# Optimization experiments

Measured on AMD Instinct MI355X. Metric: run time of the kernel, lower is better.

Reference implementation:

```python
import jax, jax.numpy as jnp
import numpy as np

SIGMA = 1.0
EPS = 1e-5
NEG = 0.1
CPG = 16  # channels_per_group


def bn(x, g, b):
    # batch norm over the point dimension (training-mode batch stats)
    m = x.mean(0, keepdims=True)
    v = x.var(0, keepdims=True)
    return (x - m) / jnp.sqrt(v + EPS) * g + b


def lrelu(x):
    return jnp.where(x >= 0, x, NEG * x)


def kpinv_conv(q_pts, s_pts, x, idx, kp, w_g1, b_g1, w_g2, b_g2):
    # KPInv: neighbor gather + kernel-point influence weighting + dynamically
    # generated (involution-style) per-point, per-kernel, per-group weights.
    M, H = idx.shape
    K = kp.shape[0]
    C = x.shape[1]
    G = C // CPG
    # shadow padding: far-away point, zero feature
    s_pts_p = jnp.concatenate([s_pts, jnp.full((1, s_pts.shape[1]), 1e6, s_pts.dtype)], 0)
    x_p = jnp.concatenate([x, jnp.zeros((1, C), x.dtype)], 0)
    npts = s_pts_p[idx] - q_pts[:, None, :]              # (M,H,D) relative neighbor positions
    nfeat = x_p[idx]                                      # (M,H,C) gathered neighbor features
    # squared distances to kernel points without materializing (M,H,K,D)
    d2 = ((npts ** 2).sum(-1)[:, :, None]
          + (kp ** 2).sum(-1)[None, None, :]
          - 2.0 * jnp.einsum('mhd,kd->mhk', npts, kp))    # (M,H,K)
    # linear influence, sum aggregation
    infl = jnp.clip(1.0 - jnp.sqrt(jnp.maximum(d2, 0.0)) / SIGMA, 0.0, None)
    fk = jnp.einsum('mhk,mhc->mkc', infl, nfeat)          # (M,K,C) per-kernel aggregated feats
    # generate conv weights from local max-pooled center feature
    center = jnp.max(nfeat, axis=1)                       # (M,C)
    w = lrelu(center @ w_g1 + b_g1) @ w_g2 + b_g2         # (M,K*G)
    w = w.reshape(M, K, G)
    fk = fk.reshape(M, K, G, CPG)
    return jnp.einsum('mkg,mkgc->mgc', w, fk).reshape(M, C)


def setup_inputs() -> dict:
    key = jax.random.key(0)
    ks = jax.random.split(key, 10)
    M, H, Cin, Cmid, K, D = 50000, 32, 128, 32, 15, 3
    R = 2.5
    pts = jax.random.uniform(ks[0], (M, D), dtype=jnp.float32) * 10.0
    return dict(
        q_pts=pts,
        s_pts=pts,
        s_feats=jax.random.normal(ks[1], (M, Cin), dtype=jnp.float32),
        neighbor_indices=jax.random.randint(ks[2], (M, H), 0, M),
        kernel_points=jax.random.normal(ks[3], (K, D), dtype=jnp.float32) * (0.3 * R),
        w_u1=jax.random.normal(ks[4], (Cin, Cmid), dtype=jnp.float32) / np.float32(np.sqrt(Cin)),
        g_u1=jnp.ones((Cmid,), jnp.float32), b_u1=jnp.zeros((Cmid,), jnp.float32),
        w_g1=jax.random.normal(ks[5], (Cmid, Cmid // 4), dtype=jnp.float32) / np.float32(np.sqrt(Cmid)),
        b_g1=jnp.zeros((Cmid // 4,), jnp.float32),
        w_g2=jax.random.normal(ks[6], (Cmid // 4, K * (Cmid // CPG)), dtype=jnp.float32) / np.float32(np.sqrt(Cmid // 4)),
        b_g2=jnp.zeros((K * (Cmid // CPG),), jnp.float32),
        g_c=jnp.ones((Cmid,), jnp.float32), b_c=jnp.zeros((Cmid,), jnp.float32),
        w_u2=jax.random.normal(ks[7], (Cmid, Cin), dtype=jnp.float32) / np.float32(np.sqrt(Cmid)),
        g_u2=jnp.ones((Cin,), jnp.float32), b_u2=jnp.zeros((Cin,), jnp.float32),
    )


def reference(q_pts, s_pts, s_feats, neighbor_indices, kernel_points,
              w_u1, g_u1, b_u1, w_g1, b_g1, w_g2, b_g2,
              g_c, b_c, w_u2, g_u2, b_u2):
    # unary1: linear -> BN -> LeakyReLU (in_channels != mid_channels)
    x = lrelu(bn(s_feats @ w_u1, g_u1, b_u1))
    # KPInv conv block: conv -> BN -> LeakyReLU
    x = kpinv_conv(q_pts, s_pts, x, neighbor_indices, kernel_points, w_g1, b_g1, w_g2, b_g2)
    x = lrelu(bn(x, g_c, b_c))
    # unary2: linear -> BN (no activation)
    x = bn(x @ w_u2, g_u2, b_u2)
    # not strided, in==out: shortcut is identity on s_feats
    return lrelu(x + s_feats)
```

## Files before the change

kernel.cpp:

```cpp
#include <hip/hip_runtime.h>

#define CMID 32
#define CIN 128
#define HNB 32
#define KP 15
#define NEG 0.1f
#define EPS 1e-5f

__global__ __launch_bounds__(256) void k1_gemm1(
    const float* __restrict__ A,
    const float* __restrict__ B,
    float* __restrict__ y1,
    float* __restrict__ st,
    int M)
{
    __shared__ __align__(16) float AsT[32 * 128];
    __shared__ __align__(16) float Bs[128 * 32];
    __shared__ __align__(16) float red[256];
    int t = threadIdx.x;
    for (int i = t; i < 128 * 32; i += 256) Bs[i] = B[i];

    int m0 = blockIdx.x * 128;
    int tx = t & 7, ty = t >> 3;
    int srow = t & 127, shh = t >> 7;
    float acc[4][4] = {{0.f}};

    for (int ch = 0; ch < 4; ++ch) {
        __syncthreads();
        int gr = m0 + srow;
        const float4* ap = (const float4*)(A + (size_t)gr * CIN + ch * 32 + shh * 16);
        float4 f0, f1, f2, f3;
        if (gr < M) { f0 = ap[0]; f1 = ap[1]; f2 = ap[2]; f3 = ap[3]; }
        else { f0 = f1 = f2 = f3 = make_float4(0.f, 0.f, 0.f, 0.f); }
        {
            int cb = shh * 16;
            AsT[(cb + 0) * 128 + srow] = f0.x;  AsT[(cb + 1) * 128 + srow] = f0.y;
            AsT[(cb + 2) * 128 + srow] = f0.z;  AsT[(cb + 3) * 128 + srow] = f0.w;
            AsT[(cb + 4) * 128 + srow] = f1.x;  AsT[(cb + 5) * 128 + srow] = f1.y;
            AsT[(cb + 6) * 128 + srow] = f1.z;  AsT[(cb + 7) * 128 + srow] = f1.w;
            AsT[(cb + 8) * 128 + srow] = f2.x;  AsT[(cb + 9) * 128 + srow] = f2.y;
            AsT[(cb + 10) * 128 + srow] = f2.z; AsT[(cb + 11) * 128 + srow] = f2.w;
            AsT[(cb + 12) * 128 + srow] = f3.x; AsT[(cb + 13) * 128 + srow] = f3.y;
            AsT[(cb + 14) * 128 + srow] = f3.z; AsT[(cb + 15) * 128 + srow] = f3.w;
        }
        __syncthreads();
        const float* bsp = Bs + (ch * 32) * 32 + tx * 4;
#pragma unroll
        for (int jl = 0; jl < 32; ++jl) {
            float4 av = *(const float4*)(AsT + jl * 128 + ty * 4);
            float4 bv = *(const float4*)(bsp + jl * 32);
            acc[0][0] += av.x * bv.x; acc[0][1] += av.x * bv.y; acc[0][2] += av.x * bv.z; acc[0][3] += av.x * bv.w;
            acc[1][0] += av.y * bv.x; acc[1][1] += av.y * bv.y; acc[1][2] += av.y * bv.z; acc[1][3] += av.y * bv.w;
            acc[2][0] += av.z * bv.x; acc[2][1] += av.z * bv.y; acc[2][2] += av.z * bv.z; acc[2][3] += av.z * bv.w;
            acc[3][0] += av.w * bv.x; acc[3][1] += av.w * bv.y; acc[3][2] += av.w * bv.z; acc[3][3] += av.w * bv.w;
        }
    }
#pragma unroll
    for (int i = 0; i < 4; ++i) {
        int r = m0 + ty * 4 + i;
        if (r < M)
            *(float4*)(y1 + (size_t)r * CMID + tx * 4) =
                make_float4(acc[i][0], acc[i][1], acc[i][2], acc[i][3]);
    }
    float s4[4], q4[4];
#pragma unroll
    for (int e = 0; e < 4; ++e) {
        s4[e] = acc[0][e] + acc[1][e] + acc[2][e] + acc[3][e];
        q4[e] = acc[0][e] * acc[0][e] + acc[1][e] * acc[1][e]
              + acc[2][e] * acc[2][e] + acc[3][e] * acc[3][e];
    }
#pragma unroll
    for (int off = 8; off <= 32; off <<= 1) {
#pragma unroll
        for (int e = 0; e < 4; ++e) {
            s4[e] += __shfl_xor(s4[e], off);
            q4[e] += __shfl_xor(q4[e], off);
        }
    }
    int lw = t >> 6, ll = t & 63;
    if (ll < 8) {
#pragma unroll
        for (int e = 0; e < 4; ++e) {
            red[(lw * 8 + ll) * 8 + e] = s4[e];
            red[(lw * 8 + ll) * 8 + 4 + e] = q4[e];
        }
    }
    __syncthreads();
    if (t < 64) {
        int tx2 = t >> 3, k = t & 7;
        float v = red[(0 * 8 + tx2) * 8 + k] + red[(1 * 8 + tx2) * 8 + k]
                + red[(2 * 8 + tx2) * 8 + k] + red[(3 * 8 + tx2) * 8 + k];
        int col = tx2 * 4 + (k & 3);
        atomicAdd(&st[(k < 4 ? 0 : 32) + col], v);
    }
}

__global__ __launch_bounds__(256, 4) void k3_kpinv(
    const float* __restrict__ y1, const float* __restrict__ st,
    const float* __restrict__ q_pts, const float* __restrict__ s_pts,
    const int* __restrict__ idx, const float* __restrict__ kp,
    const float* __restrict__ g_u1, const float* __restrict__ b_u1,
    const float* __restrict__ w_g1, const float* __restrict__ b_g1,
    const float* __restrict__ w_g2, const float* __restrict__ b_g2,
    float* __restrict__ x2, int M)
{
    __shared__ __align__(16) float a1s[32], b1s[32];
    __shared__ __align__(16) float wg1[32 * 8];
    __shared__ __align__(16) float bg1[8];
    __shared__ __align__(16) float wg2[8 * 30];
    __shared__ __align__(16) float bg2[32];
    __shared__ __align__(16) float kps[KP * 3 + 1];
    __shared__ __align__(16) float vbuf[4][2][32 * 32];
    __shared__ __align__(16) float aux[4][2][144];

    int t = threadIdx.x;
    if (t < 32) {
        float mean = st[t] * (1.0f / M);
        float var  = st[32 + t] * (1.0f / M) - mean * mean;
        float inv  = rsqrtf(var + EPS);
        float a = g_u1[t] * inv;
        a1s[t] = a;
        b1s[t] = b_u1[t] - mean * a;
    }
    wg1[t & 255] = w_g1[t & 255];
    if (t < 8)   bg1[t] = b_g1[t];
    if (t < 240) wg2[t] = w_g2[t];
    if (t < 30)  bg2[t] = b_g2[t];
    else if (t < 32) bg2[t] = 0.f;
    if (t < KP * 3) kps[t] = kp[t];
    __syncthreads();

    int wave = t >> 6, lane = t & 63;
    int p = lane >> 5;
    int q = lane & 31;
    int m = blockIdx.x * 8 + wave * 2 + p;
    bool valid = (m < M);
    int mm = valid ? m : 0;
    float* vb = &vbuf[wave][p][0];
    float* ax = &aux[wave][p][0];

    int h = q;
    int n = idx[(size_t)mm * HNB + h];
    float qx = q_pts[mm * 3 + 0], qy = q_pts[mm * 3 + 1], qz = q_pts[mm * 3 + 2];
    float dx = s_pts[n * 3 + 0] - qx;
    float dy = s_pts[n * 3 + 1] - qy;
    float dz = s_pts[n * 3 + 2] - qz;

    float infl[KP];
#pragma unroll
    for (int k = 0; k < KP; ++k) {
        float ex = dx - kps[k * 3 + 0];
        float ey = dy - kps[k * 3 + 1];
        float ez = dz - kps[k * 3 + 2];
        float d = sqrtf(ex * ex + ey * ey + ez * ez);
        infl[k] = fmaxf(1.0f - d, 0.f);
    }

    {
        const float4* row = (const float4*)(y1 + (size_t)n * CMID);
        int hq4 = h >> 2, h3 = h & 3;
#pragma unroll
        for (int jj = 0; jj < 8; ++jj) {
            float4 f = row[jj];
            float vv[4] = {f.x, f.y, f.z, f.w};
#pragma unroll
            for (int e = 0; e < 4; ++e) {
                int c = jj * 4 + e;
                float x = vv[e] * a1s[c] + b1s[c];
                x = fmaxf(x, NEG * x);
                vb[(c << 5) + ((hq4 ^ (c & 7)) << 2) + h3] = x;
            }
        }
    }
    __builtin_amdgcn_wave_barrier();

    {
        int c = q;
        int c7 = c & 7;
        const float* vrow = vb + (c << 5);
        float cm = -1e30f;
#pragma unroll
        for (int j = 0; j < 8; ++j) {
            const float4 f = *(const float4*)(vrow + ((j ^ c7) << 2));
            cm = fmaxf(fmaxf(fmaxf(cm, f.x), fmaxf(f.y, f.z)), f.w);
        }
        ax[c] = cm;
        __builtin_amdgcn_wave_barrier();

        int jm = c & 7;
        float acc = bg1[jm];
#pragma unroll
        for (int cc = 0; cc < 8; ++cc) {
            const float4 ce = *(const float4*)(ax + (cc << 2));
            acc += ce.x * wg1[(cc * 4 + 0) * 8 + jm];
            acc += ce.y * wg1[(cc * 4 + 1) * 8 + jm];
            acc += ce.z * wg1[(cc * 4 + 2) * 8 + jm];
            acc += ce.w * wg1[(cc * 4 + 3) * 8 + jm];
        }
        float h1v = fmaxf(acc, NEG * acc);
        if (c < 8) ax[32 + c] = h1v;
        __builtin_amdgcn_wave_barrier();

        float wv = 0.f;
        if (c < 30) {
            const float4 ha = *(const float4*)(ax + 32);
            const float4 hb = *(const float4*)(ax + 36);
            wv = bg2[c]
               + ha.x * wg2[0 * 30 + c] + ha.y * wg2[1 * 30 + c]
               + ha.z * wg2[2 * 30 + c] + ha.w * wg2[3 * 30 + c]
               + hb.x * wg2[4 * 30 + c] + hb.y * wg2[5 * 30 + c]
               + hb.z * wg2[6 * 30 + c] + hb.w * wg2[7 * 30 + c];
        }
        ax[40 + c] = wv;
    }
    __builtin_amdgcn_wave_barrier();

    {
        float wf[32];
#pragma unroll
        for (int j = 0; j < 8; ++j) {
            const float4 wc = *(const float4*)(ax + 40 + (j << 2));
            wf[j * 4 + 0] = wc.x; wf[j * 4 + 1] = wc.y;
            wf[j * 4 + 2] = wc.z; wf[j * 4 + 3] = wc.w;
        }
        float s0 = 0.f, s1 = 0.f;
#pragma unroll
        for (int k = 0; k < KP; ++k) {
            s0 += infl[k] * wf[2 * k + 0];
            s1 += infl[k] * wf[2 * k + 1];
        }
        ax[72 + q]  = s0;
        ax[104 + q] = s1;
    }
    __builtin_amdgcn_wave_barrier();

    {
        int c = q;
        int c7 = c & 7;
        const float* sbuf = ax + 72 + ((c >> 4) << 5);
        const float* vrow = vb + (c << 5);
        float o = 0.f;
#pragma unroll
        for (int j = 0; j < 8; ++j) {
            const float4 vv = *(const float4*)(vrow + ((j ^ c7) << 2));
            const float4 ss = *(const float4*)(sbuf + (j << 2));
            o += vv.x * ss.x + vv.y * ss.y + vv.z * ss.z + vv.w * ss.w;
        }
        if (valid) x2[(size_t)m * CMID + c] = o;
    }
}

__global__ __launch_bounds__(256) void k4_stats32(
    const float* __restrict__ x2, float* __restrict__ st, int M)
{
    int t = threadIdx.x;
    int c = t & 31;
    float sum = 0.f, sq = 0.f;
    for (int r = blockIdx.x * 8 + (t >> 5); r < M; r += gridDim.x * 8) {
        float v = x2[(size_t)r * CMID + c];
        sum += v; sq += v * v;
    }
    __shared__ float red[256];
    red[t] = sum; __syncthreads();
    if (t < 32) { float s = 0.f; for (int i = 0; i < 8; ++i) s += red[t + 32 * i]; atomicAdd(&st[64 + t], s); }
    __syncthreads();
    red[t] = sq; __syncthreads();
    if (t < 32) { float s = 0.f; for (int i = 0; i < 8; ++i) s += red[t + 32 * i]; atomicAdd(&st[96 + t], s); }
}

__global__ __launch_bounds__(256) void k6_zstats(
    const float* __restrict__ x2, const float* __restrict__ w_u2,
    const float* __restrict__ g_c, const float* __restrict__ b_c,
    float* __restrict__ st, int M)
{
    __shared__ __align__(16) float ST[32 * 128];
    __shared__ __align__(16) float Ws[32 * 32];
    __shared__ __align__(16) float acs[32], bcs[32];
    __shared__ __align__(16) float red[256];
    int t = threadIdx.x;
    int cb = blockIdx.y;
    int m0 = blockIdx.x * 128;
    if (t < 32) {
        float mean = st[64 + t] * (1.0f / M);
        float var  = st[96 + t] * (1.0f / M) - mean * mean;
        float inv  = rsqrtf(var + EPS);
        float a = g_c[t] * inv;
        acs[t] = a; bcs[t] = b_c[t] - mean * a;
    }
    for (int i = t; i < 32 * 32; i += 256)
        Ws[i] = w_u2[(i >> 5) * CIN + cb * 32 + (i & 31)];
    __syncthreads();

    int srow = t & 127, shh = t >> 7;
    int gr = m0 + srow;
    const float4* xp = (const float4*)(x2 + (size_t)gr * CMID + shh * 16);
    float4 f0, f1, f2, f3;
    if (gr < M) { f0 = xp[0]; f1 = xp[1]; f2 = xp[2]; f3 = xp[3]; }
    else { f0 = f1 = f2 = f3 = make_float4(0.f, 0.f, 0.f, 0.f); }
    {
        float vv[16] = {f0.x, f0.y, f0.z, f0.w, f1.x, f1.y, f1.z, f1.w,
                        f2.x, f2.y, f2.z, f2.w, f3.x, f3.y, f3.z, f3.w};
        int cbse = shh * 16;
#pragma unroll
        for (int e = 0; e < 16; ++e) {
            int c = cbse + e;
            float x = vv[e] * acs[c] + bcs[c];
            x = fmaxf(x, NEG * x);
            ST[c * 128 + srow] = (gr < M) ? x : 0.f;
        }
    }
    __syncthreads();

    int tx = t & 7, ty = t >> 3;
    float acc[4][4] = {{0.f}};
#pragma unroll
    for (int j = 0; j < 32; ++j) {
        float4 av = *(const float4*)(ST + j * 128 + ty * 4);
        float4 bv = *(const float4*)(Ws + j * 32 + tx * 4);
        acc[0][0] += av.x * bv.x; acc[0][1] += av.x * bv.y; acc[0][2] += av.x * bv.z; acc[0][3] += av.x * bv.w;
        acc[1][0] += av.y * bv.x; acc[1][1] += av.y * bv.y; acc[1][2] += av.y * bv.z; acc[1][3] += av.y * bv.w;
        acc[2][0] += av.z * bv.x; acc[2][1] += av.z * bv.y; acc[2][2] += av.z * bv.z; acc[2][3] += av.z * bv.w;
        acc[3][0] += av.w * bv.x; acc[3][1] += av.w * bv.y; acc[3][2] += av.w * bv.z; acc[3][3] += av.w * bv.w;
    }
    float s4[4], q4[4];
#pragma unroll
    for (int e = 0; e < 4; ++e) {
        s4[e] = acc[0][e] + acc[1][e] + acc[2][e] + acc[3][e];
        q4[e] = acc[0][e] * acc[0][e] + acc[1][e] * acc[1][e]
              + acc[2][e] * acc[2][e] + acc[3][e] * acc[3][e];
    }
#pragma unroll
    for (int off = 8; off <= 32; off <<= 1) {
#pragma unroll
        for (int e = 0; e < 4; ++e) {
            s4[e] += __shfl_xor(s4[e], off);
            q4[e] += __shfl_xor(q4[e], off);
        }
    }
    int lw = t >> 6, ll = t & 63;
    if (ll < 8) {
#pragma unroll
        for (int e = 0; e < 4; ++e) {
            red[(lw * 8 + ll) * 8 + e] = s4[e];
            red[(lw * 8 + ll) * 8 + 4 + e] = q4[e];
        }
    }
    __syncthreads();
    if (t < 64) {
        int tx2 = t >> 3, k = t & 7;
        float v = red[(0 * 8 + tx2) * 8 + k] + red[(1 * 8 + tx2) * 8 + k]
                + red[(2 * 8 + tx2) * 8 + k] + red[(3 * 8 + tx2) * 8 + k];
        int col = cb * 32 + tx2 * 4 + (k & 3);
        atomicAdd(&st[(k < 4 ? 128 : 256) + col], v);
    }
}

__global__ __launch_bounds__(256) void k8_final(
    const float* __restrict__ x2, const float* __restrict__ w_u2,
    const float* __restrict__ g_c, const float* __restrict__ b_c,
    const float* __restrict__ g_u2, const float* __restrict__ b_u2,
    const float* __restrict__ s_feats, const float* __restrict__ st,
    float* __restrict__ out, int M)
{
    __shared__ __align__(16) float ST[32 * 128];
    __shared__ __align__(16) float Ws[32 * 32];
    __shared__ __align__(16) float acs[32], bcs[32];
    __shared__ __align__(16) float a2s[32], b2s[32];
    int t = threadIdx.x;
    int cb = blockIdx.y;
    int m0 = blockIdx.x * 128;
    if (t < 32) {
        float mean = st[64 + t] * (1.0f / M);
        float var  = st[96 + t] * (1.0f / M) - mean * mean;
        float inv  = rsqrtf(var + EPS);
        float a = g_c[t] * inv;
        acs[t] = a; bcs[t] = b_c[t] - mean * a;
        int c = cb * 32 + t;
        float mean2 = st[128 + c] * (1.0f / M);
        float var2  = st[256 + c] * (1.0f / M) - mean2 * mean2;
        float inv2  = rsqrtf(var2 + EPS);
        float a2 = g_u2[c] * inv2;
        a2s[t] = a2; b2s[t] = b_u2[c] - mean2 * a2;
    }
    for (int i = t; i < 32 * 32; i += 256)
        Ws[i] = w_u2[(i >> 5) * CIN + cb * 32 + (i & 31)];
    __syncthreads();

    int srow = t & 127, shh = t >> 7;
    int gr = m0 + srow;
    const float4* xp = (const float4*)(x2 + (size_t)gr * CMID + shh * 16);
    float4 f0, f1, f2, f3;
    if (gr < M) { f0 = xp[0]; f1 = xp[1]; f2 = xp[2]; f3 = xp[3]; }
    else { f0 = f1 = f2 = f3 = make_float4(0.f, 0.f, 0.f, 0.f); }
    {
        float vv[16] = {f0.x, f0.y, f0.z, f0.w, f1.x, f1.y, f1.z, f1.w,
                        f2.x, f2.y, f2.z, f2.w, f3.x, f3.y, f3.z, f3.w};
        int cbse = shh * 16;
#pragma unroll
        for (int e = 0; e < 16; ++e) {
            int c = cbse + e;
            float x = vv[e] * acs[c] + bcs[c];
            x = fmaxf(x, NEG * x);
            ST[c * 128 + srow] = (gr < M) ? x : 0.f;
        }
    }
    __syncthreads();

    int tx = t & 7, ty = t >> 3;
    float acc[4][4] = {{0.f}};
#pragma unroll
    for (int j = 0; j < 32; ++j) {
        float4 av = *(const float4*)(ST + j * 128 + ty * 4);
        float4 bv = *(const float4*)(Ws + j * 32 + tx * 4);
        acc[0][0] += av.x * bv.x; acc[0][1] += av.x * bv.y; acc[0][2] += av.x * bv.z; acc[0][3] += av.x * bv.w;
        acc[1][0] += av.y * bv.x; acc[1][1] += av.y * bv.y; acc[1][2] += av.y * bv.z; acc[1][3] += av.y * bv.w;
        acc[2][0] += av.z * bv.x; acc[2][1] += av.z * bv.y; acc[2][2] += av.z * bv.z; acc[2][3] += av.z * bv.w;
        acc[3][0] += av.w * bv.x; acc[3][1] += av.w * bv.y; acc[3][2] += av.w * bv.z; acc[3][3] += av.w * bv.w;
    }
    int lc = tx * 4;
    float a0 = a2s[lc + 0], a1 = a2s[lc + 1], a2v = a2s[lc + 2], a3 = a2s[lc + 3];
    float bb0 = b2s[lc + 0], bb1 = b2s[lc + 1], bb2 = b2s[lc + 2], bb3 = b2s[lc + 3];
#pragma unroll
    for (int i = 0; i < 4; ++i) {
        int r = m0 + ty * 4 + i;
        if (r < M) {
            size_t gi = (size_t)r * CIN + cb * 32 + lc;
            float4 sf = *(const float4*)(s_feats + gi);
            float v0 = acc[i][0] * a0 + bb0 + sf.x;
            float v1 = acc[i][1] * a1 + bb1 + sf.y;
            float v2 = acc[i][2] * a2v + bb2 + sf.z;
            float v3 = acc[i][3] * a3 + bb3 + sf.w;
            v0 = fmaxf(v0, NEG * v0); v1 = fmaxf(v1, NEG * v1);
            v2 = fmaxf(v2, NEG * v2); v3 = fmaxf(v3, NEG * v3);
            *(float4*)(out + gi) = make_float4(v0, v1, v2, v3);
        }
    }
}

extern "C" void kernel_launch(void* const* d_in, const int* in_sizes, int n_in,
                              void* d_out, int out_size, void* d_ws, size_t ws_size,
                              hipStream_t stream) {
    const float* q_pts   = (const float*)d_in[0];
    const float* s_pts   = (const float*)d_in[1];
    const float* s_feats = (const float*)d_in[2];
    const int*   idx     = (const int*)d_in[3];
    const float* kp      = (const float*)d_in[4];
    const float* w_u1    = (const float*)d_in[5];
    const float* g_u1    = (const float*)d_in[6];
    const float* b_u1    = (const float*)d_in[7];
    const float* w_g1    = (const float*)d_in[8];
    const float* b_g1    = (const float*)d_in[9];
    const float* w_g2    = (const float*)d_in[10];
    const float* b_g2    = (const float*)d_in[11];
    const float* g_c     = (const float*)d_in[12];
    const float* b_c     = (const float*)d_in[13];
    const float* w_u2    = (const float*)d_in[14];
    const float* g_u2    = (const float*)d_in[15];
    const float* b_u2    = (const float*)d_in[16];

    int M = in_sizes[3] / HNB;

    float* ws = (float*)d_ws;
    float* y1 = ws;
    float* x2 = ws + (size_t)M * CMID;
    float* st = ws + (size_t)M * 2 * CMID;

    hipMemsetAsync(st, 0, 384 * sizeof(float), stream);

    int nbr = (M + 127) / 128;
    k1_gemm1<<<nbr, 256, 0, stream>>>(s_feats, w_u1, y1, st, M);
    k3_kpinv<<<(M + 7) / 8, 256, 0, stream>>>(y1, st, q_pts, s_pts, idx, kp,
                                              g_u1, b_u1, w_g1, b_g1, w_g2, b_g2,
                                              x2, M);
    k4_stats32<<<128, 256, 0, stream>>>(x2, st, M);
    k6_zstats<<<dim3(nbr, 4), 256, 0, stream>>>(x2, w_u2, g_c, b_c, st, M);
    k8_final<<<dim3(nbr, 4), 256, 0, stream>>>(x2, w_u2, g_c, b_c, g_u2, b_u2,
                                               s_feats, st, (float*)d_out, M);
}
```

Baseline: 253.0 us.

## Fuse conv BN stats into kpinv kernel and store GEMM output for elementwise finish

The separate stats kernel over x2 is removed; per-block channel sums and squares are reduced in shared memory at the end of the kpinv kernel and added atomically. The z-stats GEMM kernel now also writes its pre-norm output into the output buffer, so the final kernel becomes a grid-stride elementwise BN+residual+LeakyReLU pass instead of recomputing the 32x128 GEMM. This trades one launch and a GEMM recompute for extra global writes/reads of the full output and many more atomics from the large kpinv grid.

Measured after the change: 333.0 us. +31.6%, slower.

```diff
diff --git a/kernel.cpp b/kernel.cpp
--- a/kernel.cpp
+++ b/kernel.cpp
@@ -8,11 +8,8 @@
 #define EPS 1e-5f
 
 __global__ __launch_bounds__(256) void k1_gemm1(
-    const float* __restrict__ A,
-    const float* __restrict__ B,
-    float* __restrict__ y1,
-    float* __restrict__ st,
-    int M)
+    const float* __restrict__ A, const float* __restrict__ B,
+    float* __restrict__ y1, float* __restrict__ st, int M)
 {
     __shared__ __align__(16) float AsT[32 * 128];
     __shared__ __align__(16) float Bs[128 * 32];
@@ -96,7 +93,7 @@
 }
 
 __global__ __launch_bounds__(256, 4) void k3_kpinv(
-    const float* __restrict__ y1, const float* __restrict__ st,
+    const float* __restrict__ y1, float* __restrict__ st,
     const float* __restrict__ q_pts, const float* __restrict__ s_pts,
     const int* __restrict__ idx, const float* __restrict__ kp,
     const float* __restrict__ g_u1, const float* __restrict__ b_u1,
@@ -110,7 +107,7 @@
     __shared__ __align__(16) float wg2[8 * 30];
     __shared__ __align__(16) float bg2[32];
     __shared__ __align__(16) float kps[KP * 3 + 1];
-    __shared__ __align__(16) float vbuf[4][2][32 * 32];
+    __shared__ __align__(16) float vbuf[4][2][1024];
     __shared__ __align__(16) float aux[4][2][144];
 
     int t = threadIdx.x;
@@ -138,6 +135,7 @@
     int mm = valid ? m : 0;
     float* vb = &vbuf[wave][p][0];
     float* ax = &aux[wave][p][0];
+    float osum = 0.f;
 
     int h = q;
     int n = idx[(size_t)mm * HNB + h];
@@ -246,32 +244,37 @@
             const float4 ss = *(const float4*)(sbuf + (j << 2));
             o += vv.x * ss.x + vv.y * ss.y + vv.z * ss.z + vv.w * ss.w;
         }
-        if (valid) x2[(size_t)m * CMID + c] = o;
-    }
-}
-
-__global__ __launch_bounds__(256) void k4_stats32(
-    const float* __restrict__ x2, float* __restrict__ st, int M)
-{
-    int t = threadIdx.x;
-    int c = t & 31;
-    float sum = 0.f, sq = 0.f;
-    for (int r = blockIdx.x * 8 + (t >> 5); r < M; r += gridDim.x * 8) {
-        float v = x2[(size_t)r * CMID + c];
-        sum += v; sq += v * v;
-    }
-    __shared__ float red[256];
-    red[t] = sum; __syncthreads();
-    if (t < 32) { float s = 0.f; for (int i = 0; i < 8; ++i) s += red[t + 32 * i]; atomicAdd(&st[64 + t], s); }
-    __syncthreads();
-    red[t] = sq; __syncthreads();
-    if (t < 32) { float s = 0.f; for (int i = 0; i < 8; ++i) s += red[t + 32 * i]; atomicAdd(&st[96 + t], s); }
+        if (valid) {
+            x2[(size_t)m * CMID + c] = o;
+            osum = o;
+        }
+    }
+
+    __syncthreads();
+    float* red = &vbuf[0][0][0];
+    red[t] = osum;
+    __syncthreads();
+    if (t < 32) {
+        float s = 0.f;
+#pragma unroll
+        for (int i = 0; i < 8; ++i) s += red[t + 32 * i];
+        atomicAdd(&st[64 + t], s);
+    }
+    __syncthreads();
+    red[t] = osum * osum;
+    __syncthreads();
+    if (t < 32) {
+        float s = 0.f;
+#pragma unroll
+        for (int i = 0; i < 8; ++i) s += red[t + 32 * i];
+        atomicAdd(&st[96 + t], s);
+    }
 }
 
 __global__ __launch_bounds__(256) void k6_zstats(
     const float* __restrict__ x2, const float* __restrict__ w_u2,
     const float* __restrict__ g_c, const float* __restrict__ b_c,
-    float* __restrict__ st, int M)
+    float* __restrict__ st, float* __restrict__ zout, int M)
 {
     __shared__ __align__(16) float ST[32 * 128];
     __shared__ __align__(16) float Ws[32 * 32];
@@ -322,6 +325,13 @@
         acc[2][0] += av.z * bv.x; acc[2][1] += av.z * bv.y; acc[2][2] += av.z * bv.z; acc[2][3] += av.z * bv.w;
         acc[3][0] += av.w * bv.x; acc[3][1] += av.w * bv.y; acc[3][2] += av.w * bv.z; acc[3][3] += av.w * bv.w;
     }
+#pragma unroll
+    for (int i = 0; i < 4; ++i) {
+        int r = m0 + ty * 4 + i;
+        if (r < M)
+            *(float4*)(zout + (size_t)r * CIN + cb * 32 + tx * 4) =
+                make_float4(acc[i][0], acc[i][1], acc[i][2], acc[i][3]);
+    }
     float s4[4], q4[4];
 #pragma unroll
     for (int e = 0; e < 4; ++e) {
@@ -355,85 +365,36 @@
     }
 }
 
-__global__ __launch_bounds__(256) void k8_final(
-    const float* __restrict__ x2, const float* __restrict__ w_u2,
-    const float* __restrict__ g_c, const float* __restrict__ b_c,
+__global__ __launch_bounds__(256) void k8_elem(
+    const float* __restrict__ s_feats,
     const float* __restrict__ g_u2, const float* __restrict__ b_u2,
-    const float* __restrict__ s_feats, const float* __restrict__ st,
-    float* __restrict__ out, int M)
+    const float* __restrict__ st, float* __restrict__ out, int M)
 {
-    __shared__ __align__(16) float ST[32 * 128];
-    __shared__ __align__(16) float Ws[32 * 32];
-    __shared__ __align__(16) float acs[32], bcs[32];
-    __shared__ __align__(16) float a2s[32], b2s[32];
+    __shared__ float a2s[128], b2s[128];
     int t = threadIdx.x;
-    int cb = blockIdx.y;
-    int m0 = blockIdx.x * 128;
-    if (t < 32) {
-        float mean = st[64 + t] * (1.0f / M);
-        float var  = st[96 + t] * (1.0f / M) - mean * mean;
+    if (t < 128) {
+        float mean = st[128 + t] * (1.0f / M);
+        float var  = st[256 + t] * (1.0f / M) - mean * mean;
         float inv  = rsqrtf(var + EPS);
-        float a = g_c[t] * inv;
-        acs[t] = a; bcs[t] = b_c[t] - mean * a;
-        int c = cb * 32 + t;
-        float mean2 = st[128 + c] * (1.0f / M);
-        float var2  = st[256 + c] * (1.0f / M) - mean2 * mean2;
-        float inv2  = rsqrtf(var2 + EPS);
-        float a2 = g_u2[c] * inv2;
-        a2s[t] = a2; b2s[t] = b_u2[c] - mean2 * a2;
-    }
-    for (int i = t; i < 32 * 32; i += 256)
-        Ws[i] = w_u2[(i >> 5) * CIN + cb * 32 + (i & 31)];
-    __syncthreads();
-
-    int srow = t & 127, shh = t >> 7;
-    int gr = m0 + srow;
-    const float4* xp = (const float4*)(x2 + (size_t)gr * CMID + shh * 16);
-    float4 f0, f1, f2, f3;
-    if (gr < M) { f0 = xp[0]; f1 = xp[1]; f2 = xp[2]; f3 = xp[3]; }
-    else { f0 = f1 = f2 = f3 = make_float4(0.f, 0.f, 0.f, 0.f); }
-    {
-        float vv[16] = {f0.x, f0.y, f0.z, f0.w, f1.x, f1.y, f1.z, f1.w,
-                        f2.x, f2.y, f2.z, f2.w, f3.x, f3.y, f3.z, f3.w};
-        int cbse = shh * 16;
-#pragma unroll
-        for (int e = 0; e < 16; ++e) {
-            int c = cbse + e;
-            float x = vv[e] * acs[c] + bcs[c];
-            x = fmaxf(x, NEG * x);
-            ST[c * 128 + srow] = (gr < M) ? x : 0.f;
-        }
-    }
-    __syncthreads();
-
-    int tx = t & 7, ty = t >> 3;
-    float acc[4][4] = {{0.f}};
-#pragma unroll
-    for (int j = 0; j < 32; ++j) {
-        float4 av = *(const float4*)(ST + j * 128 + ty * 4);
-        float4 bv = *(const float4*)(Ws + j * 32 + tx * 4);
-        acc[0][0] += av.x * bv.x; acc[0][1] += av.x * bv.y; acc[0][2] += av.x * bv.z; acc[0][3] += av.x * bv.w;
-        acc[1][0] += av.y * bv.x; acc[1][1] += av.y * bv.y; acc[1][2] += av.y * bv.z; acc[1][3] += av.y * bv.w;
-        acc[2][0] += av.z * bv.x; acc[2][1] += av.z * bv.y; acc[2][2] += av.z * bv.z; acc[2][3] += av.z * bv.w;
-        acc[3][0] += av.w * bv.x; acc[3][1] += av.w * bv.y; acc[3][2] += av.w * bv.z; acc[3][3] += av.w * bv.w;
-    }
-    int lc = tx * 4;
-    float a0 = a2s[lc + 0], a1 = a2s[lc + 1], a2v = a2s[lc + 2], a3 = a2s[lc + 3];
-    float bb0 = b2s[lc + 0], bb1 = b2s[lc + 1], bb2 = b2s[lc + 2], bb3 = b2s[lc + 3];
-#pragma unroll
-    for (int i = 0; i < 4; ++i) {
-        int r = m0 + ty * 4 + i;
-        if (r < M) {
-            size_t gi = (size_t)r * CIN + cb * 32 + lc;
-            float4 sf = *(const float4*)(s_feats + gi);
-            float v0 = acc[i][0] * a0 + bb0 + sf.x;
-            float v1 = acc[i][1] * a1 + bb1 + sf.y;
-            float v2 = acc[i][2] * a2v + bb2 + sf.z;
-            float v3 = acc[i][3] * a3 + bb3 + sf.w;
-            v0 = fmaxf(v0, NEG * v0); v1 = fmaxf(v1, NEG * v1);
-            v2 = fmaxf(v2, NEG * v2); v3 = fmaxf(v3, NEG * v3);
-            *(float4*)(out + gi) = make_float4(v0, v1, v2, v3);
-        }
+        float a = g_u2[t] * inv;
+        a2s[t] = a; b2s[t] = b_u2[t] - mean * a;
+    }
+    __syncthreads();
+    size_t total = (size_t)M * 32;
+    float4* o4 = (float4*)out;
+    const float4* s4 = (const float4*)s_feats;
+    for (size_t i = (size_t)blockIdx.x * 256 + t; i < total;
+         i += (size_t)gridDim.x * 256) {
+        float4 z = o4[i];
+        float4 sf = s4[i];
+        int c = ((int)(i & 31)) * 4;
+        float v0 = z.x * a2s[c + 0] + b2s[c + 0] + sf.x;
+        float v1 = z.y * a2s[c + 1] + b2s[c + 1] + sf.y;
+        float v2 = z.z * a2s[c + 2] + b2s[c + 2] + sf.z;
+        float v3 = z.w * a2s[c + 3] + b2s[c + 3] + sf.w;
+        v0 = fmaxf(v0, NEG * v0); v1 = fmaxf(v1, NEG * v1);
+        v2 = fmaxf(v2, NEG * v2); v3 = fmaxf(v3, NEG * v3);
+        o4[i] = make_float4(v0, v1, v2, v3);
     }
 }
 
@@ -464,6 +425,7 @@
     float* y1 = ws;
     float* x2 = ws + (size_t)M * CMID;
     float* st = ws + (size_t)M * 2 * CMID;
+    float* out = (float*)d_out;
 
     hipMemsetAsync(st, 0, 384 * sizeof(float), stream);
 
@@ -472,8 +434,6 @@
     k3_kpinv<<<(M + 7) / 8, 256, 0, stream>>>(y1, st, q_pts, s_pts, idx, kp,
                                               g_u1, b_u1, w_g1, b_g1, w_g2, b_g2,
                                               x2, M);
-    k4_stats32<<<128, 256, 0, stream>>>(x2, st, M);
-    k6_zstats<<<dim3(nbr, 4), 256, 0, stream>>>(x2, w_u2, g_c, b_c, st, M);
-    k8_final<<<dim3(nbr, 4), 256, 0, stream>>>(x2, w_u2, g_c, b_c, g_u2, b_u2,
-                                               s_feats, st, (float*)d_out, M);
+    k6_zstats<<<dim3(nbr, 4), 256, 0, stream>>>(x2, w_u2, g_c, b_c, st, out, M);
+    k8_elem<<<2048, 256, 0, stream>>>(s_feats, g_u2, b_u2, st, out, M);
 }
```
